# Optimization experiments

Measured on AMD Instinct MI355X. Metric: run time of the kernel, lower is better.

Reference implementation:

```python
import jax, jax.numpy as jnp
import numpy as np

N = 10000
E = 40000
C_IN = 32
C_HID = 64
C_OUT = 32
C_E_IN = 16
C_E_HID = 128


def _edge_mlp(eattr, w1, b1, w2, b2):
    # edge_NN: Linear -> ReLU -> Linear -> ReLU
    h = jax.nn.relu(eattr @ w1 + b1)
    return jax.nn.relu(h @ w2 + b2)


def _nnconv(x, src, dst, eattr, w1, b1, w2, b2, root, bias, c_in, c_out):
    # per-edge weight matrices [E, c_in, c_out]
    w = _edge_mlp(eattr, w1, b1, w2, b2).reshape(-1, c_in, c_out)
    # gather source node features and apply per-edge matmul
    msg = jnp.einsum('ei,eio->eo', x[src], w)  # [E, c_out]
    aggr = jax.ops.segment_sum(msg, dst, num_segments=N)  # sum aggregation
    return aggr + x @ root + bias  # root weight + bias (NNConv defaults)


def setup_inputs() -> dict:
    key = jax.random.key(0)
    ks = jax.random.split(key, 16)
    s = 0.1  # small init scale to keep activations bounded through ReLUs
    inp = {
        'x': jax.random.normal(ks[0], (N, C_IN), dtype=jnp.float32),
        'edge_index': jax.random.randint(ks[1], (2, E), 0, N, dtype=jnp.int64) if jax.config.jax_enable_x64 else jax.random.randint(ks[1], (2, E), 0, N, dtype=jnp.int32),
        'edge_attr': jax.random.uniform(ks[2], (E, C_E_IN), dtype=jnp.float32),
        # layer 1 (c_in=32 -> c_hidden=64)
        'l1_ew1': jax.random.normal(ks[3], (C_E_IN, C_E_HID), dtype=jnp.float32) * s,
        'l1_eb1': jnp.zeros((C_E_HID,), dtype=jnp.float32),
        'l1_ew2': jax.random.normal(ks[4], (C_E_HID, C_IN * C_HID), dtype=jnp.float32) * s,
        'l1_eb2': jnp.zeros((C_IN * C_HID,), dtype=jnp.float32),
        'l1_root': jax.random.normal(ks[5], (C_IN, C_HID), dtype=jnp.float32) * s,
        'l1_bias': jnp.zeros((C_HID,), dtype=jnp.float32),
        # layer 2 (c_hidden=64 -> c_out=32)
        'l2_ew1': jax.random.normal(ks[6], (C_E_IN, C_E_HID), dtype=jnp.float32) * s,
        'l2_eb1': jnp.zeros((C_E_HID,), dtype=jnp.float32),
        'l2_ew2': jax.random.normal(ks[7], (C_E_HID, C_HID * C_OUT), dtype=jnp.float32) * s,
        'l2_eb2': jnp.zeros((C_HID * C_OUT,), dtype=jnp.float32),
        'l2_root': jax.random.normal(ks[8], (C_HID, C_OUT), dtype=jnp.float32) * s,
        'l2_bias': jnp.zeros((C_OUT,), dtype=jnp.float32),
    }
    return inp


def reference(x, edge_index, edge_attr,
              l1_ew1, l1_eb1, l1_ew2, l1_eb2, l1_root, l1_bias,
              l2_ew1, l2_eb1, l2_ew2, l2_eb2, l2_root, l2_bias):
    src, dst = edge_index[0], edge_index[1]
    h = _nnconv(x, src, dst, edge_attr, l1_ew1, l1_eb1, l1_ew2, l1_eb2,
                l1_root, l1_bias, C_IN, C_HID)
    h = jax.nn.relu(h)  # dropout is identity in eval mode
    out = _nnconv(h, src, dst, edge_attr, l2_ew1, l2_eb1, l2_ew2, l2_eb2,
                  l2_root, l2_bias, C_HID, C_OUT)
    return out
```

## Files before the change

### kernel.cpp

```cpp
#include <hip/hip_runtime.h>

#define NN 10000
#define NE 40000

typedef __attribute__((ext_vector_type(8))) short bf16x8;
typedef __attribute__((ext_vector_type(4))) float f32x4;
typedef __attribute__((ext_vector_type(8))) unsigned short u16x8;

__device__ inline unsigned short bf16rne(float f) {
  union { float f; unsigned u; } v; v.f = f;
  return (unsigned short)((v.u + 0x7FFFu + ((v.u >> 16) & 1u)) >> 16);
}

__global__ void k_reorder2(const float* __restrict__ e1, const float* __restrict__ e2,
                           unsigned short* __restrict__ o1, unsigned short* __restrict__ o2) {
  const float* ew2 = (blockIdx.x < 128) ? e1 : e2;
  unsigned short* out = (blockIdx.x < 128) ? o1 : o2;
  const int ct = blockIdx.x & 127;
  const int l  = threadIdx.x & 63;
  const int kk = threadIdx.x >> 6;
  const int col = ct * 16 + (l & 15);
  const int g = l >> 4;
  u16x8 v;
#pragma unroll
  for (int j = 0; j < 8; ++j) v[j] = bf16rne(ew2[(kk * 32 + g * 8 + j) * 2048 + col]);
  *reinterpret_cast<u16x8*>(out + ((size_t)(ct * 2048 + kk * 512 + l * 8))) = v;
}

__global__ void k_reorder_e2(const float* __restrict__ e1, const float* __restrict__ e2,
                             unsigned short* __restrict__ o1, unsigned short* __restrict__ o2) {
  const float* ew1 = blockIdx.x ? e2 : e1;
  unsigned short* out = blockIdx.x ? o2 : o1;
  const int l  = threadIdx.x & 63;
  const int ct = threadIdx.x >> 6;
  const int g = l >> 4;
  u16x8 v;
#pragma unroll
  for (int j = 0; j < 8; ++j) {
    int k = g * 8 + j;
    v[j] = (k < 16) ? bf16rne(ew1[k * 128 + ct * 16 + (l & 15)]) : (unsigned short)0;
  }
  *reinterpret_cast<u16x8*>(out + ((size_t)(ct * 64 + l) * 8)) = v;
}

template <int KI, int KO, bool RELU_IN>
__global__ void k_root(const float* __restrict__ xin, const float* __restrict__ root,
                       const float* __restrict__ bias, float* __restrict__ out) {
  int idx = blockIdx.x * 256 + threadIdx.x;
  if (idx >= NN * KO) return;
  int n = idx / KO, o = idx % KO;
  float acc = bias[o];
#pragma unroll
  for (int k = 0; k < KI; ++k) {
    float v = xin[n * KI + k];
    if (RELU_IN) v = fmaxf(v, 0.f);
    acc += v * root[k * KO + o];
  }
  out[idx] = acc;
}

template <int CI, int CO, bool RELU_IN>
__global__ __launch_bounds__(256, 2) void k_edge(
    const int* __restrict__ src, const int* __restrict__ dst,
    const float* __restrict__ eattr,
    const unsigned short* __restrict__ ew1f, const float* __restrict__ eb1,
    const unsigned short* __restrict__ bfrag, const float* __restrict__ eb2,
    const float* __restrict__ xin, float* __restrict__ aggr) {
  constexpr int TE = 64;
  const int tid = threadIdx.x;
  const int e0 = blockIdx.x * TE;
  const int toff = blockIdx.x & 31;

  __shared__ int s_src[TE];
  __shared__ int s_dst[TE];
  __shared__ float s_x[CI][68];
  __shared__ unsigned short s_hfrag[16 * 64 * 8];

  if (tid < TE) { s_src[tid] = src[e0 + tid]; s_dst[tid] = dst[e0 + tid]; }
  __syncthreads();

  for (int idx = tid; idx < TE * CI; idx += 256) {
    int e = idx / CI, c = idx % CI;
    float v = xin[(size_t)s_src[e] * CI + c];
    if (RELU_IN) v = fmaxf(v, 0.f);
    s_x[c][e] = v;
  }

  const int l = tid & 63, w = tid >> 6, g = l >> 4, c16 = l & 15;

  {
    const int m = w;
    bf16x8 ea;
#pragma unroll
    for (int j = 0; j < 8; ++j) ea[j] = 0;
    if (g < 2) {
      const float* p = eattr + (size_t)(e0 + 16 * m + c16) * 16 + g * 8;
      f32x4 v0 = *reinterpret_cast<const f32x4*>(p);
      f32x4 v1 = *reinterpret_cast<const f32x4*>(p + 4);
#pragma unroll
      for (int j = 0; j < 4; ++j) { ea[j] = bf16rne(v0[j]); ea[4 + j] = bf16rne(v1[j]); }
    }
#pragma unroll
    for (int ct = 0; ct < 8; ++ct) {
      bf16x8 bw = *reinterpret_cast<const bf16x8*>(ew1f + (size_t)(ct * 64 + l) * 8);
      const float bb = eb1[ct * 16 + c16];
      f32x4 acc = {bb, bb, bb, bb};
      acc = __builtin_amdgcn_mfma_f32_16x16x32_bf16(ea, bw, acc, 0, 0, 0);
#pragma unroll
      for (int r = 0; r < 4; ++r) {
        const int c = ct * 16 + c16;
        s_hfrag[(((m * 4) + (c >> 5)) * 64 + ((c >> 3) & 3) * 16 + g * 4 + r) * 8 + (c & 7)] =
            bf16rne(fmaxf(acc[r], 0.f));
      }
    }
  }
  __syncthreads();

  bf16x8 afrag[4][4];
#pragma unroll
  for (int m = 0; m < 4; ++m)
#pragma unroll
    for (int kk = 0; kk < 4; ++kk)
      afrag[m][kk] = *reinterpret_cast<const bf16x8*>(&s_hfrag[((m * 4 + kk) * 64 + l) * 8]);

  float msg[4][4];
#pragma unroll
  for (int m = 0; m < 4; ++m)
#pragma unroll
    for (int r = 0; r < 4; ++r) msg[m][r] = 0.f;

  const int ocol = (CI == 32) ? (w * 16 + c16) : ((w & 1) * 16 + c16);
  const bf16x8* Bb = reinterpret_cast<const bf16x8*>(bfrag);

  bf16x8 bA[4], bB[4];

#define PREF(T, BUF)                                                             \
  {                                                                              \
    const int tt_ = ((T) + toff) & 31;                                           \
    const int i_ = (CI == 32) ? tt_ : ((w >> 1) + 2 * tt_);                      \
    const int ct_ = (CI == 32) ? (tt_ * 4 + w) : (i_ * 2 + (w & 1));             \
    const bf16x8* bp_ = Bb + (size_t)ct_ * 256 + l;                              \
    _Pragma("unroll") for (int kk = 0; kk < 4; ++kk) BUF[kk] = bp_[kk * 64];     \
  }

#define COMP(T, BUF)                                                             \
  {                                                                              \
    const int tt_ = ((T) + toff) & 31;                                           \
    const int i_ = (CI == 32) ? tt_ : ((w >> 1) + 2 * tt_);                      \
    const float bb = eb2[i_ * CO + ocol];                                        \
    __builtin_amdgcn_s_setprio(1);                                               \
    _Pragma("unroll") for (int m = 0; m < 4; ++m) {                              \
      f32x4 wacc = {0.f, 0.f, 0.f, 0.f};                                         \
      _Pragma("unroll") for (int kk = 0; kk < 4; ++kk)                           \
          wacc = __builtin_amdgcn_mfma_f32_16x16x32_bf16(afrag[m][kk], BUF[kk],  \
                                                         wacc, 0, 0, 0);         \
      const f32x4 xs = *reinterpret_cast<const f32x4*>(&s_x[i_][m * 16 + g * 4]);\
      _Pragma("unroll") for (int r = 0; r < 4; ++r)                              \
          msg[m][r] += fmaxf(wacc[r] + bb, 0.f) * xs[r];                         \
    }                                                                            \
    __builtin_amdgcn_s_setprio(0);                                               \
  }

  PREF(0, bA)
#pragma unroll 1
  for (int t = 0; t < 30; t += 2) {
    PREF(t + 1, bB)
    COMP(t, bA)
    PREF(t + 2, bA)
    COMP(t + 1, bB)
  }
  PREF(31, bB)
  COMP(30, bA)
  COMP(31, bB)
#undef PREF
#undef COMP

#pragma unroll
  for (int m = 0; m < 4; ++m)
#pragma unroll
    for (int r = 0; r < 4; ++r)
      atomicAdd(&aggr[(size_t)s_dst[m * 16 + g * 4 + r] * CO + ocol], msg[m][r]);
}

extern "C" void kernel_launch(void* const* d_in, const int* in_sizes, int n_in,
                              void* d_out, int out_size, void* d_ws, size_t ws_size,
                              hipStream_t stream) {
  const float* x       = (const float*)d_in[0];
  const int*   ei      = (const int*)d_in[1];
  const float* eattr   = (const float*)d_in[2];
  const float* l1_ew1  = (const float*)d_in[3];
  const float* l1_eb1  = (const float*)d_in[4];
  const float* l1_ew2  = (const float*)d_in[5];
  const float* l1_eb2  = (const float*)d_in[6];
  const float* l1_root = (const float*)d_in[7];
  const float* l1_bias = (const float*)d_in[8];
  const float* l2_ew1  = (const float*)d_in[9];
  const float* l2_eb1  = (const float*)d_in[10];
  const float* l2_ew2  = (const float*)d_in[11];
  const float* l2_eb2  = (const float*)d_in[12];
  const float* l2_root = (const float*)d_in[13];
  const float* l2_bias = (const float*)d_in[14];

  const int* src = ei;
  const int* dst = ei + NE;

  char* ws = (char*)d_ws;
  float* P1 = (float*)ws;
  unsigned short* B1  = (unsigned short*)(ws + 2560000);
  unsigned short* B2  = (unsigned short*)(ws + 3084288);
  unsigned short* B1e = (unsigned short*)(ws + 3608576);
  unsigned short* B2e = (unsigned short*)(ws + 3616768);
  float* outf = (float*)d_out;

  k_reorder2<<<256, 256, 0, stream>>>(l1_ew2, l2_ew2, B1, B2);
  k_reorder_e2<<<2, 512, 0, stream>>>(l1_ew1, l2_ew1, B1e, B2e);

  k_root<32, 64, false><<<(NN * 64 + 255) / 256, 256, 0, stream>>>(x, l1_root, l1_bias, P1);
  k_edge<32, 64, false><<<NE / 64, 256, 0, stream>>>(src, dst, eattr, B1e, l1_eb1, B1, l1_eb2, x, P1);
  k_root<64, 32, true><<<(NN * 32 + 255) / 256, 256, 0, stream>>>(P1, l2_root, l2_bias, outf);
  k_edge<64, 32, true><<<NE / 64, 256, 0, stream>>>(src, dst, eattr, B2e, l2_eb1, B2, l2_eb2, P1, outf);
}
```

Measured before the change: 82.83 us.

## Merge setup kernels and fold root projection into edge kernels via atomics

Combines the two weight-reorder kernels into one setup kernel that also zero-fills the intermediate and output buffers. Each layer's root projection plus bias now runs as extra blocks appended to the edge-message kernel's grid, and those blocks atomically add into the zeroed aggregation buffer. This cuts the launch count from six to three and lets the root work overlap with the edge work. In exchange it adds zero-fill writes and one extra atomic per output element, and the root blocks now contend with edge blocks for the same addresses.

New measurement: 70.21 us (median of 2 runs). 15.2% less time.

```diff
diff --git a/kernel.cpp b/kernel.cpp
--- a/kernel.cpp
+++ b/kernel.cpp
@@ -12,62 +12,80 @@
   return (unsigned short)((v.u + 0x7FFFu + ((v.u >> 16) & 1u)) >> 16);
 }
 
-__global__ void k_reorder2(const float* __restrict__ e1, const float* __restrict__ e2,
-                           unsigned short* __restrict__ o1, unsigned short* __restrict__ o2) {
-  const float* ew2 = (blockIdx.x < 128) ? e1 : e2;
-  unsigned short* out = (blockIdx.x < 128) ? o1 : o2;
-  const int ct = blockIdx.x & 127;
-  const int l  = threadIdx.x & 63;
-  const int kk = threadIdx.x >> 6;
-  const int col = ct * 16 + (l & 15);
-  const int g = l >> 4;
-  u16x8 v;
-#pragma unroll
-  for (int j = 0; j < 8; ++j) v[j] = bf16rne(ew2[(kk * 32 + g * 8 + j) * 2048 + col]);
-  *reinterpret_cast<u16x8*>(out + ((size_t)(ct * 2048 + kk * 512 + l * 8))) = v;
-}
-
-__global__ void k_reorder_e2(const float* __restrict__ e1, const float* __restrict__ e2,
-                             unsigned short* __restrict__ o1, unsigned short* __restrict__ o2) {
-  const float* ew1 = blockIdx.x ? e2 : e1;
-  unsigned short* out = blockIdx.x ? o2 : o1;
-  const int l  = threadIdx.x & 63;
-  const int ct = threadIdx.x >> 6;
-  const int g = l >> 4;
-  u16x8 v;
-#pragma unroll
-  for (int j = 0; j < 8; ++j) {
-    int k = g * 8 + j;
-    v[j] = (k < 16) ? bf16rne(ew1[k * 128 + ct * 16 + (l & 15)]) : (unsigned short)0;
-  }
-  *reinterpret_cast<u16x8*>(out + ((size_t)(ct * 64 + l) * 8)) = v;
-}
-
-template <int KI, int KO, bool RELU_IN>
-__global__ void k_root(const float* __restrict__ xin, const float* __restrict__ root,
-                       const float* __restrict__ bias, float* __restrict__ out) {
-  int idx = blockIdx.x * 256 + threadIdx.x;
-  if (idx >= NN * KO) return;
-  int n = idx / KO, o = idx % KO;
-  float acc = bias[o];
-#pragma unroll
-  for (int k = 0; k < KI; ++k) {
-    float v = xin[n * KI + k];
-    if (RELU_IN) v = fmaxf(v, 0.f);
-    acc += v * root[k * KO + o];
-  }
-  out[idx] = acc;
+__global__ void k_setup(const float* __restrict__ e1w2, const float* __restrict__ e2w2,
+                        const float* __restrict__ e1w1, const float* __restrict__ e2w1,
+                        unsigned short* __restrict__ B1, unsigned short* __restrict__ B2,
+                        unsigned short* __restrict__ B1e, unsigned short* __restrict__ B2e,
+                        float* __restrict__ P1, float* __restrict__ outf) {
+  const int b = blockIdx.x;
+  const int tid = threadIdx.x;
+  if (b < 256) {
+    const float* ew2 = (b < 128) ? e1w2 : e2w2;
+    unsigned short* out = (b < 128) ? B1 : B2;
+    const int ct = b & 127;
+    const int l = tid & 63, kk = tid >> 6, g = l >> 4;
+    const int col = ct * 16 + (l & 15);
+    u16x8 v;
+#pragma unroll
+    for (int j = 0; j < 8; ++j) v[j] = bf16rne(ew2[(kk * 32 + g * 8 + j) * 2048 + col]);
+    *reinterpret_cast<u16x8*>(out + ((size_t)(ct * 2048 + kk * 512 + l * 8))) = v;
+  } else if (b < 258) {
+    const float* ew1 = (b == 256) ? e1w1 : e2w1;
+    unsigned short* out = (b == 256) ? B1e : B2e;
+    const int l = tid & 63, g = l >> 4;
+#pragma unroll
+    for (int half = 0; half < 2; ++half) {
+      const int ct = (tid >> 6) + half * 4;
+      u16x8 v;
+#pragma unroll
+      for (int j = 0; j < 8; ++j) {
+        int k = g * 8 + j;
+        v[j] = (k < 16) ? bf16rne(ew1[k * 128 + ct * 16 + (l & 15)]) : (unsigned short)0;
+      }
+      *reinterpret_cast<u16x8*>(out + ((size_t)(ct * 64 + l) * 8)) = v;
+    }
+  } else if (b < 258 + 625) {
+    f32x4 z = {0.f, 0.f, 0.f, 0.f};
+    *reinterpret_cast<f32x4*>(&P1[(size_t)(b - 258) * 1024 + tid * 4]) = z;
+  } else {
+    const size_t idx = (size_t)(b - 883) * 1024 + tid * 4;
+    if (idx + 3 < (size_t)NN * 32) {
+      f32x4 z = {0.f, 0.f, 0.f, 0.f};
+      *reinterpret_cast<f32x4*>(&outf[idx]) = z;
+    } else {
+      for (size_t u = idx; u < (size_t)NN * 32; ++u) outf[u] = 0.f;
+    }
+  }
 }
 
 template <int CI, int CO, bool RELU_IN>
-__global__ __launch_bounds__(256, 2) void k_edge(
+__global__ __launch_bounds__(256, 2) void k_layer(
     const int* __restrict__ src, const int* __restrict__ dst,
     const float* __restrict__ eattr,
     const unsigned short* __restrict__ ew1f, const float* __restrict__ eb1,
     const unsigned short* __restrict__ bfrag, const float* __restrict__ eb2,
+    const float* __restrict__ rootw, const float* __restrict__ rootb,
     const float* __restrict__ xin, float* __restrict__ aggr) {
   constexpr int TE = 64;
+  constexpr int NEB = NE / TE;
   const int tid = threadIdx.x;
+
+  if ((int)blockIdx.x >= NEB) {
+    const int idx = ((int)blockIdx.x - NEB) * 256 + tid;
+    if (idx < NN * CO) {
+      const int n = idx / CO, o = idx % CO;
+      float acc = rootb[o];
+#pragma unroll
+      for (int k = 0; k < CI; ++k) {
+        float v = xin[(size_t)n * CI + k];
+        if (RELU_IN) v = fmaxf(v, 0.f);
+        acc += v * rootw[k * CO + o];
+      }
+      atomicAdd(&aggr[idx], acc);
+    }
+    return;
+  }
+
   const int e0 = blockIdx.x * TE;
   const int toff = blockIdx.x & 31;
 
@@ -212,11 +230,10 @@
   unsigned short* B2e = (unsigned short*)(ws + 3616768);
   float* outf = (float*)d_out;
 
-  k_reorder2<<<256, 256, 0, stream>>>(l1_ew2, l2_ew2, B1, B2);
-  k_reorder_e2<<<2, 512, 0, stream>>>(l1_ew1, l2_ew1, B1e, B2e);
-
-  k_root<32, 64, false><<<(NN * 64 + 255) / 256, 256, 0, stream>>>(x, l1_root, l1_bias, P1);
-  k_edge<32, 64, false><<<NE / 64, 256, 0, stream>>>(src, dst, eattr, B1e, l1_eb1, B1, l1_eb2, x, P1);
-  k_root<64, 32, true><<<(NN * 32 + 255) / 256, 256, 0, stream>>>(P1, l2_root, l2_bias, outf);
-  k_edge<64, 32, true><<<NE / 64, 256, 0, stream>>>(src, dst, eattr, B2e, l2_eb1, B2, l2_eb2, P1, outf);
-}
+  k_setup<<<1196, 256, 0, stream>>>(l1_ew2, l2_ew2, l1_ew1, l2_ew1,
+                                    B1, B2, B1e, B2e, P1, outf);
+  k_layer<32, 64, false><<<NE / 64 + (NN * 64 + 255) / 256, 256, 0, stream>>>(
+      src, dst, eattr, B1e, l1_eb1, B1, l1_eb2, l1_root, l1_bias, x, P1);
+  k_layer<64, 32, true><<<NE / 64 + (NN * 32 + 255) / 256, 256, 0, stream>>>(
+      src, dst, eattr, B2e, l2_eb1, B2, l2_eb2, l2_root, l2_bias, P1, outf);
+}
```
